# Optimization experiments

Measured on AMD Instinct MI355X. Metric: run time of the kernel, lower is better.

The kernel has to match this reference:

```python
import jax, jax.numpy as jnp
import numpy as np

EPS = 1e-5      # BatchNorm eps
QLEV = 255.0    # 8-bit PACT activation levels (unsigned)
WMAX = 127.0    # int8 symmetric weight range


def _ste(x, q):
    # straight-through estimator: forward value q, gradient of x
    return x + jax.lax.stop_gradient(q - x)


def _wquant(w):
    # channel-wise symmetric int8 fake-quant of conv weights (per out-channel)
    s = jnp.maximum(jnp.max(jnp.abs(w), axis=(1, 2, 3), keepdims=True) / WMAX, 1e-8)
    q = jnp.clip(jnp.round(w / s), -WMAX, WMAX) * s
    return _ste(w, q)


def _conv3x3(x, w, stride=1):
    return jax.lax.conv_general_dilated(
        x, w, window_strides=(stride, stride), padding=((1, 1), (1, 1)),
        dimension_numbers=("NCHW", "OIHW", "NCHW"))


def _bn(x, g, b, m, v):
    # folded BatchNorm: per-channel affine with running stats
    return (x - m) * (g * jax.lax.rsqrt(v + EPS)) + b


def _pact(x, alpha):
    # PACT: clip to [0, alpha] then 8-bit per-channel fake-quant
    c = jnp.clip(x, 0.0, alpha)
    s = alpha / QLEV
    q = jnp.round(c / s) * s
    return _ste(c, q)


def _requant(x, s):
    # requantize onto common grid s (shift-based align in the int model)
    return _ste(x, jnp.round(x / s) * s)


def setup_inputs() -> dict:
    key = jax.random.key(0)
    ks = jax.random.split(key, 10)
    N, C, H, W = 32, 128, 56, 56
    x = jax.random.normal(ks[0], (N, C, H, W), jnp.float32)
    w1 = jax.random.normal(ks[1], (C, C, 3, 3), jnp.float32) * 0.05
    w2 = jax.random.normal(ks[2], (C, C, 3, 3), jnp.float32) * 0.05
    pc = (1, C, 1, 1)
    g1 = jnp.ones(pc, jnp.float32); b1 = jnp.zeros(pc, jnp.float32)
    m1 = jax.random.normal(ks[3], pc, jnp.float32) * 0.1
    v1 = jax.random.uniform(ks[4], pc, jnp.float32) + 0.5
    g2 = jnp.ones(pc, jnp.float32); b2 = jnp.zeros(pc, jnp.float32)
    m2 = jax.random.normal(ks[5], pc, jnp.float32) * 0.1
    v2 = jax.random.uniform(ks[6], pc, jnp.float32) + 0.5
    a1 = jax.random.uniform(ks[7], pc, jnp.float32) * 2.0 + 2.0
    a2 = jax.random.uniform(ks[8], pc, jnp.float32) * 2.0 + 2.0
    a3 = jax.random.uniform(ks[9], pc, jnp.float32) * 2.0 + 2.0
    return {"x": x, "w1": w1, "g1": g1, "b1": b1, "m1": m1, "v1": v1, "a1": a1,
            "w2": w2, "g2": g2, "b2": b2, "m2": m2, "v2": v2, "a2": a2, "a3": a3}


def reference(x, w1, g1, b1, m1, v1, a1, w2, g2, b2, m2, v2, a2, a3):
    # branch: quant-conv -> BN -> PACT-quant, twice
    out = _pact(_bn(_conv3x3(x, _wquant(w1)), g1, b1, m1, v1), a1)
    out = _pact(_bn(_conv3x3(out, _wquant(w2)), g2, b2, m2, v2), a2)
    # shift-based residual add: align both operands to act3's quant grid, add, clip+quant
    s3 = a3 / QLEV
    y = _requant(out, s3) + _requant(x, s3)
    return _pact(y, a3)
```

## Files before the change

kernel.cpp:

```cpp
#include <hip/hip_runtime.h>
#include <cstdint>

typedef __attribute__((ext_vector_type(8))) short short8;
typedef __attribute__((ext_vector_type(4))) short short4v;
typedef __attribute__((ext_vector_type(4))) float f32x4;
typedef __attribute__((ext_vector_type(4))) int int4v;
typedef __attribute__((ext_vector_type(4))) uint32_t uint4v;

#define EPSV 1e-5f

#define IMG   3136
#define NPIX  100352
#define PADTOT 13778944
#define S1Q (8.0f/127.0f)
#define S2Q (8.0f/(127.0f*254.0f))
#define S1A (4.0f/127.0f)
#define S2A (4.0f/(127.0f*254.0f))

static __device__ __forceinline__ short f2bf(float f) {
  uint32_t u = __float_as_uint(f);
  u = (u + 0x7FFFu + ((u >> 16) & 1u)) >> 16;
  return (short)u;
}

__global__ void k_halo(char* __restrict__ xq1, char* __restrict__ xq2,
                       char* __restrict__ o1k1, char* __restrict__ o1k2) {
  int i = blockIdx.x * 256 + threadIdx.x;
  int bi = i / 58368;
  int j = i - bi * 58368;
  char* buf = (bi == 0) ? xq1 : (bi == 1) ? xq2 : (bi == 2) ? o1k1 : o1k2;
  int n = j / 1824, cid = j - n * 1824;
  const int rowc = 58 * 8;
  int chunk;
  if (cid < rowc) chunk = cid;
  else if (cid < 2 * rowc) chunk = 57 * rowc + (cid - rowc);
  else {
    int e = cid - 2 * rowc;
    int h = 1 + (e >> 4);
    int r = e & 15;
    int w = (r < 8) ? 0 : 57;
    chunk = h * rowc + w * 8 + (r & 7);
  }
  long addr = ((long)n * 26912 + chunk) * 16;
  *(uint4v*)(buf + addr) = (uint4v){0u, 0u, 0u, 0u};
}

__global__ void k_wquant(const float* __restrict__ w1, const float* __restrict__ w2,
                         int8_t* __restrict__ wj1, int8_t* __restrict__ wj2,
                         float* __restrict__ ws1, float* __restrict__ ws2) {
  int o = blockIdx.x & 127;
  bool second = blockIdx.x >= 128;
  const float* src = (second ? w2 : w1) + o * 1152;
  int8_t* wj = second ? wj2 : wj1;
  __shared__ float red[256];
  int t = threadIdx.x;
  float m = 0.f;
  for (int i = t; i < 1152; i += 256) m = fmaxf(m, fabsf(src[i]));
  red[t] = m;
  __syncthreads();
  for (int s = 128; s > 0; s >>= 1) {
    if (t < s) red[t] = fmaxf(red[t], red[t + s]);
    __syncthreads();
  }
  float s = fmaxf(red[0] / 127.0f, 1e-8f);
  if (t == 0) { if (second) ws2[o] = s; else ws1[o] = s; }
  for (int i = t; i < 1152; i += 256) {
    float q = rintf(src[i] / s);
    q = fminf(fmaxf(q, -127.f), 127.f);
    int ci = i / 9, tap = i - ci * 9;
    wj[(tap * 128 + o) * 128 + ci] = (int8_t)(int)q;
  }
}

__global__ void k_params(const float* g1, const float* b1, const float* m1, const float* v1, const float* a1,
                         const float* g2, const float* b2, const float* m2, const float* v2, const float* a2,
                         const float* a3, const float* ws1, const float* ws2,
                         f32x4* pp1, f32x4* pp2, f32x4* pp3) {
  int c = threadIdx.x;
  if (c < 128) {
    float r1 = 1.0f / sqrtf(v1[c] + EPSV);
    float sc1 = g1[c] * r1;
    pp1[c] = (f32x4){ws1[c] * sc1, b1[c] - m1[c] * sc1, 255.0f / a1[c], a1[c] / 255.0f};
    float r2 = 1.0f / sqrtf(v2[c] + EPSV);
    float sc2 = g2[c] * r2;
    pp2[c] = (f32x4){ws2[c] * sc2, b2[c] - m2[c] * sc2, 255.0f / a2[c], a2[c] / 255.0f};
    pp3[c] = (f32x4){a3[c] / 255.0f, 255.0f / a3[c], a3[c], 0.0f};
  }
}

__global__ void k_transform(const float* __restrict__ x, int8_t* __restrict__ xq1, int8_t* __restrict__ xq2) {
  int b = blockIdx.x;
  int n = b / 56, h = b - (b / 56) * 56;
  __shared__ float lds[7296];
  const float* base = x + (size_t)n * 401408 + h * 56;
  int t = threadIdx.x;
  for (int idx = t; idx < 7168; idx += 256) {
    int ci = idx / 56, w = idx - (idx / 56) * 56;
    lds[ci * 57 + w] = base[ci * 3136 + w];
  }
  __syncthreads();
  const int ob = ((n * 58 + h + 1) * 58 + 1) * 128;
  for (int idx = t; idx < 1792; idx += 256) {
    int w = idx >> 5, c4 = (idx & 31) * 4;
    uint32_t p1 = 0, p2 = 0;
#pragma unroll
    for (int j = 0; j < 4; ++j) {
      float v = lds[(c4 + j) * 57 + w];
      float j1 = rintf(v * (127.0f / 8.0f));
      j1 = fminf(fmaxf(j1, -127.f), 127.f);
      float rr = v - j1 * S1Q;
      float j2 = rintf(rr * ((127.0f * 254.0f) / 8.0f));
      j2 = fminf(fmaxf(j2, -127.f), 127.f);
      p1 |= ((uint32_t)((int)j1 & 0xff)) << (8 * j);
      p2 |= ((uint32_t)((int)j2 & 0xff)) << (8 * j);
    }
    *(uint32_t*)(xq1 + ob + w * 128 + c4) = p1;
    *(uint32_t*)(xq2 + ob + w * 128 + c4) = p2;
  }
}

__global__ __launch_bounds__(256, 2) void k_conv1(
    const int8_t* __restrict__ xq1, const int8_t* __restrict__ xq2,
    const int8_t* __restrict__ wj1, const f32x4* __restrict__ pp1,
    int8_t* __restrict__ o1k1, int8_t* __restrict__ o1k2) {
  __shared__ char smem[49152];
  char* Al = smem;
  char* Bh = smem + 16384;
  char* Bl = smem + 32768;
  const int t = threadIdx.x;
  const int l = t & 63;
  const int wv = t >> 6;
  const int wr = wv >> 1, wc = wv & 1;
  const int lane15 = l & 15, hi4 = l >> 4;
  const int px0 = blockIdx.x * 128;
  const int srow = t >> 3, sl = t & 7;

  int pixbase[4];
#pragma unroll
  for (int r = 0; r < 4; ++r) {
    unsigned gpx = px0 + srow + 32 * r;
    unsigned n = gpx / IMG;
    unsigned rem = gpx - n * IMG;
    unsigned h = rem / 56;
    unsigned w = rem - h * 56;
    pixbase[r] = (int)(((n * 58u + h) * 58u + w) * 128u) + sl * 16;
  }

  int4v acc1[4][4], acc2[4][4];
#pragma unroll
  for (int i = 0; i < 4; ++i)
#pragma unroll
    for (int j = 0; j < 4; ++j) { acc1[i][j] = (int4v){0,0,0,0}; acc2[i][j] = (int4v){0,0,0,0}; }

#pragma unroll 1
  for (int tap = 0; tap < 9; ++tap) {
    const int kh = tap / 3, kw = tap - kh * 3;
    const int tapoff = (kh * 58 + kw) * 128;
    int4v av[4], bhv[4], blv[4];
#pragma unroll
    for (int r = 0; r < 4; ++r) {
      const int row = srow + 32 * r;
      av[r]  = *(const int4v*)(wj1 + (tap * 128 + row) * 128 + sl * 16);
      bhv[r] = *(const int4v*)(xq1 + pixbase[r] + tapoff);
      blv[r] = *(const int4v*)(xq2 + pixbase[r] + tapoff);
    }
    __syncthreads();
#pragma unroll
    for (int r = 0; r < 4; ++r) {
      const int row = srow + 32 * r;
      const int ss = row * 128 + ((sl ^ (row & 7)) * 16);
      *(int4v*)&Al[ss] = av[r];
      *(int4v*)&Bh[ss] = bhv[r];
      *(int4v*)&Bl[ss] = blv[r];
    }
    __syncthreads();
#pragma unroll
    for (int kk = 0; kk < 2; ++kk) {
      int4v a[4];
#pragma unroll
      for (int m = 0; m < 4; ++m) {
        const int row = wr * 64 + m * 16 + lane15;
        a[m] = *(const int4v*)&Al[row * 128 + (((kk * 4 + hi4) ^ (row & 7)) * 16)];
      }
      int4v bv[4];
#pragma unroll
      for (int n2 = 0; n2 < 4; ++n2) {
        const int row = wc * 64 + n2 * 16 + lane15;
        bv[n2] = *(const int4v*)&Bh[row * 128 + (((kk * 4 + hi4) ^ (row & 7)) * 16)];
      }
#pragma unroll
      for (int m = 0; m < 4; ++m)
#pragma unroll
        for (int n2 = 0; n2 < 4; ++n2)
          acc1[m][n2] = __builtin_amdgcn_mfma_i32_16x16x64_i8(a[m], bv[n2], acc1[m][n2], 0, 0, 0);
#pragma unroll
      for (int n2 = 0; n2 < 4; ++n2) {
        const int row = wc * 64 + n2 * 16 + lane15;
        bv[n2] = *(const int4v*)&Bl[row * 128 + (((kk * 4 + hi4) ^ (row & 7)) * 16)];
      }
#pragma unroll
      for (int m = 0; m < 4; ++m)
#pragma unroll
        for (int n2 = 0; n2 < 4; ++n2)
          acc2[m][n2] = __builtin_amdgcn_mfma_i32_16x16x64_i8(a[m], bv[n2], acc2[m][n2], 0, 0, 0);
    }
  }

  __syncthreads();
  char* sT1 = smem;
  char* sT2 = smem + 16384;
#pragma unroll
  for (int m = 0; m < 4; ++m) {
    const int cobase = wr * 64 + m * 16 + 4 * hi4;
    const int slot = cobase >> 4, off = cobase & 15;
#pragma unroll
    for (int n2 = 0; n2 < 4; ++n2) {
      const int pxl = wc * 64 + n2 * 16 + lane15;
      uint32_t pk1 = 0, pk2 = 0;
#pragma unroll
      for (int r = 0; r < 4; ++r) {
        f32x4 p = pp1[cobase + r];
        float accf = (float)acc1[m][n2][r] * S1Q + (float)acc2[m][n2][r] * S2Q;
        float y = accf * p[0] + p[1];
        float cv = fminf(fmaxf(y, 0.f), p[3] * 255.0f);
        float act = rintf(cv * p[2]) * p[3];
        float k1 = fminf(rintf(act * (127.0f / 4.0f)), 127.f);
        float rr = act - k1 * S1A;
        float k2 = fminf(fmaxf(rintf(rr * ((127.0f * 254.0f) / 4.0f)), -127.f), 127.f);
        pk1 |= ((uint32_t)((int)k1 & 0xff)) << (8 * r);
        pk2 |= ((uint32_t)((int)k2 & 0xff)) << (8 * r);
      }
      const int ad = pxl * 128 + ((slot ^ (pxl & 7)) * 16) + off;
      *(uint32_t*)&sT1[ad] = pk1;
      *(uint32_t*)&sT2[ad] = pk2;
    }
  }
  __syncthreads();
  {
    const int pxl = t >> 1, half = t & 1;
    unsigned gpx = px0 + pxl;
    unsigned n = gpx / IMG;
    unsigned rem = gpx - n * IMG;
    unsigned h = rem / 56;
    unsigned w = rem - h * 56;
    int ob = (int)(((n * 58u + h + 1u) * 58u + (w + 1u)) * 128u) + half * 64;
#pragma unroll
    for (int i = 0; i < 4; ++i) {
      const int slot = half * 4 + i;
      const int ad = pxl * 128 + ((slot ^ (pxl & 7)) * 16);
      uint4v v1 = *(uint4v*)&sT1[ad];
      uint4v v2 = *(uint4v*)&sT2[ad];
      *(uint4v*)(o1k1 + ob + i * 16) = v1;
      *(uint4v*)(o1k2 + ob + i * 16) = v2;
    }
  }
}

__global__ __launch_bounds__(256, 2) void k_conv2(
    const int8_t* __restrict__ o1k1, const int8_t* __restrict__ o1k2,
    const int8_t* __restrict__ wj2, const f32x4* __restrict__ pp2,
    const f32x4* __restrict__ pp3, const float* __restrict__ x,
    float* __restrict__ out) {
  __shared__ char smem[49152];
  char* Al = smem;
  char* Bh = smem + 16384;
  char* Bl = smem + 32768;
  const int t = threadIdx.x;
  const int l = t & 63;
  const int wv = t >> 6;
  const int wr = wv >> 1, wc = wv & 1;
  const int lane15 = l & 15, hi4 = l >> 4;
  const int px0 = blockIdx.x * 128;
  const int srow = t >> 3, sl = t & 7;

  int pixbase[4];
#pragma unroll
  for (int r = 0; r < 4; ++r) {
    unsigned gpx = px0 + srow + 32 * r;
    unsigned n = gpx / IMG;
    unsigned rem = gpx - n * IMG;
    unsigned h = rem / 56;
    unsigned w = rem - h * 56;
    pixbase[r] = (int)(((n * 58u + h) * 58u + w) * 128u) + sl * 16;
  }

  int4v acc1[4][4], acc2[4][4];
#pragma unroll
  for (int i = 0; i < 4; ++i)
#pragma unroll
    for (int j = 0; j < 4; ++j) { acc1[i][j] = (int4v){0,0,0,0}; acc2[i][j] = (int4v){0,0,0,0}; }

#pragma unroll 1
  for (int tap = 0; tap < 9; ++tap) {
    const int kh = tap / 3, kw = tap - kh * 3;
    const int tapoff = (kh * 58 + kw) * 128;
    int4v av[4], bhv[4], blv[4];
#pragma unroll
    for (int r = 0; r < 4; ++r) {
      const int row = srow + 32 * r;
      av[r]  = *(const int4v*)(wj2 + (tap * 128 + row) * 128 + sl * 16);
      bhv[r] = *(const int4v*)(o1k1 + pixbase[r] + tapoff);
      blv[r] = *(const int4v*)(o1k2 + pixbase[r] + tapoff);
    }
    __syncthreads();
#pragma unroll
    for (int r = 0; r < 4; ++r) {
      const int row = srow + 32 * r;
      const int ss = row * 128 + ((sl ^ (row & 7)) * 16);
      *(int4v*)&Al[ss] = av[r];
      *(int4v*)&Bh[ss] = bhv[r];
      *(int4v*)&Bl[ss] = blv[r];
    }
    __syncthreads();
#pragma unroll
    for (int kk = 0; kk < 2; ++kk) {
      int4v a[4];
#pragma unroll
      for (int m = 0; m < 4; ++m) {
        const int row = wr * 64 + m * 16 + lane15;
        a[m] = *(const int4v*)&Al[row * 128 + (((kk * 4 + hi4) ^ (row & 7)) * 16)];
      }
      int4v bv[4];
#pragma unroll
      for (int n2 = 0; n2 < 4; ++n2) {
        const int row = wc * 64 + n2 * 16 + lane15;
        bv[n2] = *(const int4v*)&Bh[row * 128 + (((kk * 4 + hi4) ^ (row & 7)) * 16)];
      }
#pragma unroll
      for (int m = 0; m < 4; ++m)
#pragma unroll
        for (int n2 = 0; n2 < 4; ++n2)
          acc1[m][n2] = __builtin_amdgcn_mfma_i32_16x16x64_i8(a[m], bv[n2], acc1[m][n2], 0, 0, 0);
#pragma unroll
      for (int n2 = 0; n2 < 4; ++n2) {
        const int row = wc * 64 + n2 * 16 + lane15;
        bv[n2] = *(const int4v*)&Bl[row * 128 + (((kk * 4 + hi4) ^ (row & 7)) * 16)];
      }
#pragma unroll
      for (int m = 0; m < 4; ++m)
#pragma unroll
        for (int n2 = 0; n2 < 4; ++n2)
          acc2[m][n2] = __builtin_amdgcn_mfma_i32_16x16x64_i8(a[m], bv[n2], acc2[m][n2], 0, 0, 0);
    }
  }

#pragma unroll
  for (int n2 = 0; n2 < 4; ++n2) {
    unsigned gpx = px0 + wc * 64 + n2 * 16 + lane15;
    unsigned n = gpx / IMG;
    unsigned rem = gpx - n * IMG;
    unsigned h = rem / 56;
    unsigned w = rem - h * 56;
    int base = (int)(n * 401408u + h * 56u + w);
#pragma unroll
    for (int m = 0; m < 4; ++m) {
      int cobase = wr * 64 + m * 16 + 4 * hi4;
#pragma unroll
      for (int r = 0; r < 4; ++r) {
        int co = cobase + r;
        f32x4 p2 = pp2[co];
        f32x4 p3 = pp3[co];
        int off = base + co * 3136;
        float accf = (float)acc1[m][n2][r] * S1A + (float)acc2[m][n2][r] * S2A;
        float y = accf * p2[0] + p2[1];
        float cv = fminf(fmaxf(y, 0.f), p2[3] * 255.0f);
        float act = rintf(cv * p2[2]) * p2[3];
        float ro = rintf(act * p3[1]) * p3[0];
        float rx = rintf(x[off] * p3[1]) * p3[0];
        float y3 = ro + rx;
        float c3 = fminf(fmaxf(y3, 0.f), p3[2]);
        out[off] = rintf(c3 * p3[1]) * p3[0];
      }
    }
  }
}

extern "C" void kernel_launch(void* const* d_in, const int* in_sizes, int n_in,
                              void* d_out, int out_size, void* d_ws, size_t ws_size,
                              hipStream_t stream) {
  (void)in_sizes; (void)n_in; (void)out_size; (void)ws_size;
  const float* x  = (const float*)d_in[0];
  const float* w1 = (const float*)d_in[1];
  const float* g1 = (const float*)d_in[2];
  const float* b1 = (const float*)d_in[3];
  const float* m1 = (const float*)d_in[4];
  const float* v1 = (const float*)d_in[5];
  const float* a1 = (const float*)d_in[6];
  const float* w2 = (const float*)d_in[7];
  const float* g2 = (const float*)d_in[8];
  const float* b2 = (const float*)d_in[9];
  const float* m2 = (const float*)d_in[10];
  const float* v2 = (const float*)d_in[11];
  const float* a2 = (const float*)d_in[12];
  const float* a3 = (const float*)d_in[13];

  char* ws = (char*)d_ws;
  int8_t* xq1  = (int8_t*)ws;
  int8_t* xq2  = (int8_t*)(ws + (size_t)PADTOT);
  int8_t* o1k1 = (int8_t*)(ws + 2 * (size_t)PADTOT);
  int8_t* o1k2 = (int8_t*)(ws + 3 * (size_t)PADTOT);
  int8_t* wj1  = (int8_t*)(ws + 4 * (size_t)PADTOT);
  int8_t* wj2  = (int8_t*)(ws + 4 * (size_t)PADTOT + 147456);
  float*  ws1  = (float*)(ws + 4 * (size_t)PADTOT + 2 * 147456);
  float*  ws2  = ws1 + 128;
  f32x4*  pp1  = (f32x4*)(ws2 + 128);
  f32x4*  pp2  = pp1 + 128;
  f32x4*  pp3  = pp2 + 128;

  k_halo<<<912, 256, 0, stream>>>((char*)xq1, (char*)xq2, (char*)o1k1, (char*)o1k2);
  k_wquant<<<256, 256, 0, stream>>>(w1, w2, wj1, wj2, ws1, ws2);
  k_params<<<1, 128, 0, stream>>>(g1, b1, m1, v1, a1, g2, b2, m2, v2, a2, a3, ws1, ws2, pp1, pp2, pp3);
  k_transform<<<1792, 256, 0, stream>>>(x, xq1, xq2);
  k_conv1<<<784, 256, 0, stream>>>(xq1, xq2, wj1, pp1, o1k1, o1k2);
  k_conv2<<<784, 256, 0, stream>>>(o1k1, o1k2, wj2, pp2, pp3, x, (float*)d_out);
}
```

Before: 149.9 us.

## Merge prep kernels, prefetch next tap, coalesce conv2 epilogue via LDS

Folds halo zeroing, weight quantization, parameter folding and input transform into one k_prep launch. The per-channel scale is now recomputed serially inside the params block, so that block no longer waits for the wquant blocks. Both conv kernels load the next tap's global tiles into registers while the current tap computes. conv2's epilogue stages accumulators through LDS so each thread writes two adjacent pixels per channel as coalesced float2 stores. When workspace allows, it reads a precomputed int16 requantized residual instead of the float input, which adds extra stores in prep and a serial 1152-element loop per params thread.

```diff
diff --git a/kernel.cpp b/kernel.cpp
--- a/kernel.cpp
+++ b/kernel.cpp
@@ -1,9 +1,8 @@
 #include <hip/hip_runtime.h>
 #include <cstdint>
 
-typedef __attribute__((ext_vector_type(8))) short short8;
-typedef __attribute__((ext_vector_type(4))) short short4v;
 typedef __attribute__((ext_vector_type(4))) float f32x4;
+typedef __attribute__((ext_vector_type(2))) float f32x2;
 typedef __attribute__((ext_vector_type(4))) int int4v;
 typedef __attribute__((ext_vector_type(4))) uint32_t uint4v;
 
@@ -17,105 +16,115 @@
 #define S1A (4.0f/127.0f)
 #define S2A (4.0f/(127.0f*254.0f))
 
-static __device__ __forceinline__ short f2bf(float f) {
-  uint32_t u = __float_as_uint(f);
-  u = (u + 0x7FFFu + ((u >> 16) & 1u)) >> 16;
-  return (short)u;
-}
-
-__global__ void k_halo(char* __restrict__ xq1, char* __restrict__ xq2,
-                       char* __restrict__ o1k1, char* __restrict__ o1k2) {
-  int i = blockIdx.x * 256 + threadIdx.x;
-  int bi = i / 58368;
-  int j = i - bi * 58368;
-  char* buf = (bi == 0) ? xq1 : (bi == 1) ? xq2 : (bi == 2) ? o1k1 : o1k2;
-  int n = j / 1824, cid = j - n * 1824;
-  const int rowc = 58 * 8;
-  int chunk;
-  if (cid < rowc) chunk = cid;
-  else if (cid < 2 * rowc) chunk = 57 * rowc + (cid - rowc);
-  else {
-    int e = cid - 2 * rowc;
-    int h = 1 + (e >> 4);
-    int r = e & 15;
-    int w = (r < 8) ? 0 : 57;
-    chunk = h * rowc + w * 8 + (r & 7);
-  }
-  long addr = ((long)n * 26912 + chunk) * 16;
-  *(uint4v*)(buf + addr) = (uint4v){0u, 0u, 0u, 0u};
-}
-
-__global__ void k_wquant(const float* __restrict__ w1, const float* __restrict__ w2,
-                         int8_t* __restrict__ wj1, int8_t* __restrict__ wj2,
-                         float* __restrict__ ws1, float* __restrict__ ws2) {
-  int o = blockIdx.x & 127;
-  bool second = blockIdx.x >= 128;
-  const float* src = (second ? w2 : w1) + o * 1152;
-  int8_t* wj = second ? wj2 : wj1;
-  __shared__ float red[256];
-  int t = threadIdx.x;
-  float m = 0.f;
-  for (int i = t; i < 1152; i += 256) m = fmaxf(m, fabsf(src[i]));
-  red[t] = m;
-  __syncthreads();
-  for (int s = 128; s > 0; s >>= 1) {
-    if (t < s) red[t] = fmaxf(red[t], red[t + s]);
-    __syncthreads();
-  }
-  float s = fmaxf(red[0] / 127.0f, 1e-8f);
-  if (t == 0) { if (second) ws2[o] = s; else ws1[o] = s; }
-  for (int i = t; i < 1152; i += 256) {
-    float q = rintf(src[i] / s);
-    q = fminf(fmaxf(q, -127.f), 127.f);
-    int ci = i / 9, tap = i - ci * 9;
-    wj[(tap * 128 + o) * 128 + ci] = (int8_t)(int)q;
-  }
-}
-
-__global__ void k_params(const float* g1, const float* b1, const float* m1, const float* v1, const float* a1,
-                         const float* g2, const float* b2, const float* m2, const float* v2, const float* a2,
-                         const float* a3, const float* ws1, const float* ws2,
-                         f32x4* pp1, f32x4* pp2, f32x4* pp3) {
-  int c = threadIdx.x;
-  if (c < 128) {
-    float r1 = 1.0f / sqrtf(v1[c] + EPSV);
-    float sc1 = g1[c] * r1;
-    pp1[c] = (f32x4){ws1[c] * sc1, b1[c] - m1[c] * sc1, 255.0f / a1[c], a1[c] / 255.0f};
-    float r2 = 1.0f / sqrtf(v2[c] + EPSV);
-    float sc2 = g2[c] * r2;
-    pp2[c] = (f32x4){ws2[c] * sc2, b2[c] - m2[c] * sc2, 255.0f / a2[c], a2[c] / 255.0f};
-    pp3[c] = (f32x4){a3[c] / 255.0f, 255.0f / a3[c], a3[c], 0.0f};
-  }
-}
-
-__global__ void k_transform(const float* __restrict__ x, int8_t* __restrict__ xq1, int8_t* __restrict__ xq2) {
-  int b = blockIdx.x;
-  int n = b / 56, h = b - (b / 56) * 56;
-  __shared__ float lds[7296];
-  const float* base = x + (size_t)n * 401408 + h * 56;
-  int t = threadIdx.x;
-  for (int idx = t; idx < 7168; idx += 256) {
-    int ci = idx / 56, w = idx - (idx / 56) * 56;
-    lds[ci * 57 + w] = base[ci * 3136 + w];
-  }
-  __syncthreads();
-  const int ob = ((n * 58 + h + 1) * 58 + 1) * 128;
-  for (int idx = t; idx < 1792; idx += 256) {
-    int w = idx >> 5, c4 = (idx & 31) * 4;
-    uint32_t p1 = 0, p2 = 0;
-#pragma unroll
-    for (int j = 0; j < 4; ++j) {
-      float v = lds[(c4 + j) * 57 + w];
-      float j1 = rintf(v * (127.0f / 8.0f));
-      j1 = fminf(fmaxf(j1, -127.f), 127.f);
-      float rr = v - j1 * S1Q;
-      float j2 = rintf(rr * ((127.0f * 254.0f) / 8.0f));
-      j2 = fminf(fmaxf(j2, -127.f), 127.f);
-      p1 |= ((uint32_t)((int)j1 & 0xff)) << (8 * j);
-      p2 |= ((uint32_t)((int)j2 & 0xff)) << (8 * j);
-    }
-    *(uint32_t*)(xq1 + ob + w * 128 + c4) = p1;
-    *(uint32_t*)(xq2 + ob + w * 128 + c4) = p2;
+__global__ __launch_bounds__(256) void k_prep(
+    const float* __restrict__ x, const float* __restrict__ w1, const float* __restrict__ w2,
+    const float* __restrict__ g1, const float* __restrict__ b1, const float* __restrict__ m1,
+    const float* __restrict__ v1, const float* __restrict__ a1,
+    const float* __restrict__ g2, const float* __restrict__ b2, const float* __restrict__ m2,
+    const float* __restrict__ v2, const float* __restrict__ a2, const float* __restrict__ a3,
+    int8_t* __restrict__ xq1, int8_t* __restrict__ xq2,
+    int8_t* __restrict__ wj1, int8_t* __restrict__ wj2,
+    char* __restrict__ o1k1, char* __restrict__ o1k2,
+    f32x4* __restrict__ pp1, f32x4* __restrict__ pp2, f32x4* __restrict__ pp3,
+    short* __restrict__ j3, int use_j3) {
+  __shared__ float shf[7296];
+  const int bid = blockIdx.x;
+  const int t = threadIdx.x;
+
+  if (bid < 1792) {
+    int n = bid / 56, h = bid - (bid / 56) * 56;
+    const float* base = x + (size_t)n * 401408 + h * 56;
+    for (int idx = t; idx < 7168; idx += 256) {
+      int ci = idx / 56, w = idx - (idx / 56) * 56;
+      shf[ci * 57 + w] = base[ci * 3136 + w];
+    }
+    __syncthreads();
+    const int ob = ((n * 58 + h + 1) * 58 + 1) * 128;
+    for (int idx = t; idx < 1792; idx += 256) {
+      int w = idx >> 5, c4 = (idx & 31) * 4;
+      uint32_t p1 = 0, p2 = 0;
+#pragma unroll
+      for (int j = 0; j < 4; ++j) {
+        float v = shf[(c4 + j) * 57 + w];
+        float j1 = rintf(v * (127.0f / 8.0f));
+        j1 = fminf(fmaxf(j1, -127.f), 127.f);
+        float rr = v - j1 * S1Q;
+        float j2 = rintf(rr * ((127.0f * 254.0f) / 8.0f));
+        j2 = fminf(fmaxf(j2, -127.f), 127.f);
+        p1 |= ((uint32_t)((int)j1 & 0xff)) << (8 * j);
+        p2 |= ((uint32_t)((int)j2 & 0xff)) << (8 * j);
+      }
+      *(uint32_t*)(xq1 + ob + w * 128 + c4) = p1;
+      *(uint32_t*)(xq2 + ob + w * 128 + c4) = p2;
+    }
+    if (use_j3) {
+      const size_t jb = (size_t)n * 401408 + h * 56;
+      for (int idx = t; idx < 7168; idx += 256) {
+        int ci = idx / 56, w = idx - (idx / 56) * 56;
+        float inv3 = 255.0f / a3[ci];
+        j3[jb + ci * 3136 + w] = (short)(int)rintf(shf[ci * 57 + w] * inv3);
+      }
+    }
+  } else if (bid < 1792 + 912) {
+    int i = (bid - 1792) * 256 + t;
+    int bi = i / 58368;
+    int j = i - bi * 58368;
+    char* buf = (bi == 0) ? (char*)xq1 : (bi == 1) ? (char*)xq2 : (bi == 2) ? o1k1 : o1k2;
+    int n = j / 1824, cid = j - n * 1824;
+    const int rowc = 58 * 8;
+    int chunk;
+    if (cid < rowc) chunk = cid;
+    else if (cid < 2 * rowc) chunk = 57 * rowc + (cid - rowc);
+    else {
+      int e = cid - 2 * rowc;
+      int h = 1 + (e >> 4);
+      int r = e & 15;
+      int w = (r < 8) ? 0 : 57;
+      chunk = h * rowc + w * 8 + (r & 7);
+    }
+    long addr = ((long)n * 26912 + chunk) * 16;
+    *(uint4v*)(buf + addr) = (uint4v){0u, 0u, 0u, 0u};
+  } else if (bid < 1792 + 912 + 256) {
+    int sub = bid - 2704;
+    int o = sub & 127;
+    bool second = sub >= 128;
+    const float* src = (second ? w2 : w1) + o * 1152;
+    int8_t* wj = second ? wj2 : wj1;
+    float* red = shf;
+    float m = 0.f;
+    for (int i = t; i < 1152; i += 256) m = fmaxf(m, fabsf(src[i]));
+    red[t] = m;
+    __syncthreads();
+    for (int s = 128; s > 0; s >>= 1) {
+      if (t < s) red[t] = fmaxf(red[t], red[t + s]);
+      __syncthreads();
+    }
+    float s = fmaxf(red[0] / 127.0f, 1e-8f);
+    for (int i = t; i < 1152; i += 256) {
+      float q = rintf(src[i] / s);
+      q = fminf(fmaxf(q, -127.f), 127.f);
+      int ci = i / 9, tap = i - ci * 9;
+      wj[(tap * 128 + o) * 128 + ci] = (int8_t)(int)q;
+    }
+  } else {
+    if (t < 128) {
+      float mx1 = 0.f, mx2 = 0.f;
+      const float* p1w = w1 + t * 1152;
+      const float* p2w = w2 + t * 1152;
+      for (int i = 0; i < 1152; ++i) {
+        mx1 = fmaxf(mx1, fabsf(p1w[i]));
+        mx2 = fmaxf(mx2, fabsf(p2w[i]));
+      }
+      float s1w = fmaxf(mx1 / 127.0f, 1e-8f);
+      float s2w = fmaxf(mx2 / 127.0f, 1e-8f);
+      float r1 = 1.0f / sqrtf(v1[t] + EPSV);
+      float sc1 = g1[t] * r1;
+      pp1[t] = (f32x4){s1w * sc1, b1[t] - m1[t] * sc1, 255.0f / a1[t], a1[t] / 255.0f};
+      float r2 = 1.0f / sqrtf(v2[t] + EPSV);
+      float sc2 = g2[t] * r2;
+      pp2[t] = (f32x4){s2w * sc2, b2[t] - m2[t] * sc2, 255.0f / a2[t], a2[t] / 255.0f};
+      pp3[t] = (f32x4){a3[t] / 255.0f, 255.0f / a3[t], a3[t], 0.0f};
+    }
   }
 }
 
@@ -152,18 +161,17 @@
 #pragma unroll
     for (int j = 0; j < 4; ++j) { acc1[i][j] = (int4v){0,0,0,0}; acc2[i][j] = (int4v){0,0,0,0}; }
 
+  int4v av[4], bhv[4], blv[4];
+#pragma unroll
+  for (int r = 0; r < 4; ++r) {
+    const int row = srow + 32 * r;
+    av[r]  = *(const int4v*)(wj1 + row * 128 + sl * 16);
+    bhv[r] = *(const int4v*)(xq1 + pixbase[r]);
+    blv[r] = *(const int4v*)(xq2 + pixbase[r]);
+  }
+
 #pragma unroll 1
   for (int tap = 0; tap < 9; ++tap) {
-    const int kh = tap / 3, kw = tap - kh * 3;
-    const int tapoff = (kh * 58 + kw) * 128;
-    int4v av[4], bhv[4], blv[4];
-#pragma unroll
-    for (int r = 0; r < 4; ++r) {
-      const int row = srow + 32 * r;
-      av[r]  = *(const int4v*)(wj1 + (tap * 128 + row) * 128 + sl * 16);
-      bhv[r] = *(const int4v*)(xq1 + pixbase[r] + tapoff);
-      blv[r] = *(const int4v*)(xq2 + pixbase[r] + tapoff);
-    }
     __syncthreads();
 #pragma unroll
     for (int r = 0; r < 4; ++r) {
@@ -174,6 +182,18 @@
       *(int4v*)&Bl[ss] = blv[r];
     }
     __syncthreads();
+    if (tap < 8) {
+      const int nt = tap + 1;
+      const int kh = nt / 3, kw = nt - kh * 3;
+      const int tapoff = (kh * 58 + kw) * 128;
+#pragma unroll
+      for (int r = 0; r < 4; ++r) {
+        const int row = srow + 32 * r;
+        av[r]  = *(const int4v*)(wj1 + (nt * 128 + row) * 128 + sl * 16);
+        bhv[r] = *(const int4v*)(xq1 + pixbase[r] + tapoff);
+        blv[r] = *(const int4v*)(xq2 + pixbase[r] + tapoff);
+      }
+    }
 #pragma unroll
     for (int kk = 0; kk < 2; ++kk) {
       int4v a[4];
@@ -260,6 +280,7 @@
     const int8_t* __restrict__ o1k1, const int8_t* __restrict__ o1k2,
     const int8_t* __restrict__ wj2, const f32x4* __restrict__ pp2,
     const f32x4* __restrict__ pp3, const float* __restrict__ x,
+    const short* __restrict__ j3, int use_j3,
     float* __restrict__ out) {
   __shared__ char smem[49152];
   char* Al = smem;
@@ -290,18 +311,17 @@
 #pragma unroll
     for (int j = 0; j < 4; ++j) { acc1[i][j] = (int4v){0,0,0,0}; acc2[i][j] = (int4v){0,0,0,0}; }
 
+  int4v av[4], bhv[4], blv[4];
+#pragma unroll
+  for (int r = 0; r < 4; ++r) {
+    const int row = srow + 32 * r;
+    av[r]  = *(const int4v*)(wj2 + row * 128 + sl * 16);
+    bhv[r] = *(const int4v*)(o1k1 + pixbase[r]);
+    blv[r] = *(const int4v*)(o1k2 + pixbase[r]);
+  }
+
 #pragma unroll 1
   for (int tap = 0; tap < 9; ++tap) {
-    const int kh = tap / 3, kw = tap - kh * 3;
-    const int tapoff = (kh * 58 + kw) * 128;
-    int4v av[4], bhv[4], blv[4];
-#pragma unroll
-    for (int r = 0; r < 4; ++r) {
-      const int row = srow + 32 * r;
-      av[r]  = *(const int4v*)(wj2 + (tap * 128 + row) * 128 + sl * 16);
-      bhv[r] = *(const int4v*)(o1k1 + pixbase[r] + tapoff);
-      blv[r] = *(const int4v*)(o1k2 + pixbase[r] + tapoff);
-    }
     __syncthreads();
 #pragma unroll
     for (int r = 0; r < 4; ++r) {
@@ -312,6 +332,18 @@
       *(int4v*)&Bl[ss] = blv[r];
     }
     __syncthreads();
+    if (tap < 8) {
+      const int nt = tap + 1;
+      const int kh = nt / 3, kw = nt - kh * 3;
+      const int tapoff = (kh * 58 + kw) * 128;
+#pragma unroll
+      for (int r = 0; r < 4; ++r) {
+        const int row = srow + 32 * r;
+        av[r]  = *(const int4v*)(wj2 + (nt * 128 + row) * 128 + sl * 16);
+        bhv[r] = *(const int4v*)(o1k1 + pixbase[r] + tapoff);
+        blv[r] = *(const int4v*)(o1k2 + pixbase[r] + tapoff);
+      }
+    }
 #pragma unroll
     for (int kk = 0; kk < 2; ++kk) {
       int4v a[4];
@@ -344,41 +376,74 @@
     }
   }
 
-#pragma unroll
-  for (int n2 = 0; n2 < 4; ++n2) {
-    unsigned gpx = px0 + wc * 64 + n2 * 16 + lane15;
-    unsigned n = gpx / IMG;
-    unsigned rem = gpx - n * IMG;
-    unsigned h = rem / 56;
-    unsigned w = rem - h * 56;
-    int base = (int)(n * 401408u + h * 56u + w);
-#pragma unroll
-    for (int m = 0; m < 4; ++m) {
-      int cobase = wr * 64 + m * 16 + 4 * hi4;
+  __syncthreads();
+  float* E = (float*)smem;
+  const int pxl2 = l * 2;
+  unsigned gpx0 = px0 + pxl2;
+  unsigned nn = gpx0 / IMG;
+  unsigned rrem = gpx0 - nn * IMG;
+  const size_t obase = (size_t)nn * 401408 + rrem;
+
+#pragma unroll 1
+  for (int m = 0; m < 4; ++m) {
+#pragma unroll
+    for (int n2 = 0; n2 < 4; ++n2) {
+      const int pxl = wc * 64 + n2 * 16 + lane15;
 #pragma unroll
       for (int r = 0; r < 4; ++r) {
-        int co = cobase + r;
-        f32x4 p2 = pp2[co];
-        f32x4 p3 = pp3[co];
-        int off = base + co * 3136;
-        float accf = (float)acc1[m][n2][r] * S1A + (float)acc2[m][n2][r] * S2A;
-        float y = accf * p2[0] + p2[1];
+        const int co_l = wr * 16 + 4 * hi4 + r;
+        E[co_l * 132 + pxl] = (float)acc1[m][n2][r] * S1A + (float)acc2[m][n2][r] * S2A;
+      }
+    }
+    __syncthreads();
+#pragma unroll 1
+    for (int cid = 0; cid < 8; ++cid) {
+      const int co_l = wv * 8 + cid;
+      const int co = m * 16 + (co_l < 16 ? co_l : co_l + 48);
+      const f32x4 p2 = pp2[co];
+      const f32x4 p3 = pp3[co];
+      const size_t off = obase + (size_t)co * 3136;
+      float v0 = E[co_l * 132 + pxl2];
+      float v1 = E[co_l * 132 + pxl2 + 1];
+      float rx0, rx1;
+      if (use_j3) {
+        const short* jp = j3 + off;
+        rx0 = (float)jp[0] * p3[0];
+        rx1 = (float)jp[1] * p3[0];
+      } else {
+        const float* xp = x + off;
+        rx0 = rintf(xp[0] * p3[1]) * p3[0];
+        rx1 = rintf(xp[1] * p3[1]) * p3[0];
+      }
+      float o0, o1;
+      {
+        float y = v0 * p2[0] + p2[1];
         float cv = fminf(fmaxf(y, 0.f), p2[3] * 255.0f);
         float act = rintf(cv * p2[2]) * p2[3];
         float ro = rintf(act * p3[1]) * p3[0];
-        float rx = rintf(x[off] * p3[1]) * p3[0];
-        float y3 = ro + rx;
+        float y3 = ro + rx0;
         float c3 = fminf(fmaxf(y3, 0.f), p3[2]);
-        out[off] = rintf(c3 * p3[1]) * p3[0];
-      }
-    }
+        o0 = rintf(c3 * p3[1]) * p3[0];
+      }
+      {
+        float y = v1 * p2[0] + p2[1];
+        float cv = fminf(fmaxf(y, 0.f), p2[3] * 255.0f);
+        float act = rintf(cv * p2[2]) * p2[3];
+        float ro = rintf(act * p3[1]) * p3[0];
+        float y3 = ro + rx1;
+        float c3 = fminf(fmaxf(y3, 0.f), p3[2]);
+        o1 = rintf(c3 * p3[1]) * p3[0];
+      }
+      *(f32x2*)(out + off) = (f32x2){o0, o1};
+    }
+    __syncthreads();
   }
 }
 
 extern "C" void kernel_launch(void* const* d_in, const int* in_sizes, int n_in,
                               void* d_out, int out_size, void* d_ws, size_t ws_size,
                               hipStream_t stream) {
-  (void)in_sizes; (void)n_in; (void)out_size; (void)ws_size;
+  (void)in_sizes; (void)n_in; (void)out_size;
   const float* x  = (const float*)d_in[0];
   const float* w1 = (const float*)d_in[1];
   const float* g1 = (const float*)d_in[2];
@@ -401,16 +466,17 @@
   int8_t* o1k2 = (int8_t*)(ws + 3 * (size_t)PADTOT);
   int8_t* wj1  = (int8_t*)(ws + 4 * (size_t)PADTOT);
   int8_t* wj2  = (int8_t*)(ws + 4 * (size_t)PADTOT + 147456);
-  float*  ws1  = (float*)(ws + 4 * (size_t)PADTOT + 2 * 147456);
-  float*  ws2  = ws1 + 128;
-  f32x4*  pp1  = (f32x4*)(ws2 + 128);
+  f32x4*  pp1  = (f32x4*)(ws + 4 * (size_t)PADTOT + 2 * 147456);
   f32x4*  pp2  = pp1 + 128;
   f32x4*  pp3  = pp2 + 128;
-
-  k_halo<<<912, 256, 0, stream>>>((char*)xq1, (char*)xq2, (char*)o1k1, (char*)o1k2);
-  k_wquant<<<256, 256, 0, stream>>>(w1, w2, wj1, wj2, ws1, ws2);
-  k_params<<<1, 128, 0, stream>>>(g1, b1, m1, v1, a1, g2, b2, m2, v2, a2, a3, ws1, ws2, pp1, pp2, pp3);
-  k_transform<<<1792, 256, 0, stream>>>(x, xq1, xq2);
+  size_t j3off = 4 * (size_t)PADTOT + 2 * 147456 + 16384;
+  short*  j3   = (short*)(ws + j3off);
+  size_t need  = j3off + (size_t)NPIX * 128 * 2;
+  int use_j3 = (ws_size >= need) ? 1 : 0;
+
+  k_prep<<<2961, 256, 0, stream>>>(x, w1, w2, g1, b1, m1, v1, a1, g2, b2, m2, v2, a2, a3,
+                                   xq1, xq2, wj1, wj2, (char*)o1k1, (char*)o1k2,
+                                   pp1, pp2, pp3, j3, use_j3);
   k_conv1<<<784, 256, 0, stream>>>(xq1, xq2, wj1, pp1, o1k1, o1k2);
-  k_conv2<<<784, 256, 0, stream>>>(o1k1, o1k2, wj2, pp2, pp3, x, (float*)d_out);
+  k_conv2<<<784, 256, 0, stream>>>(o1k1, o1k2, wj2, pp2, pp3, x, j3, use_j3, (float*)d_out);
 }
```

Measured after the change: 370.4 us. 147% more time.
